# Kernel tuning notes

Hardware: AMD Instinct MI355X
Metric: run time of the kernel (lower is better)

Reference implementation:

```python
import jax, jax.numpy as jnp
import numpy as np

H = 1024
L = 2

def setup_inputs() -> dict:
    key = jax.random.key(0)
    k1, k2, k3, k4, k5 = jax.random.split(key, 5)
    B, S = 32, 2048
    scale = 1.0 / np.sqrt(H)
    return {
        "query": jax.random.normal(k1, (B, 1, H * L), dtype=jnp.float32),
        "keys": jax.random.normal(k2, (B, S, H), dtype=jnp.float32),
        "Wa_w": jax.random.normal(k3, (H * L, H), dtype=jnp.float32) * scale,
        "Wa_b": jnp.zeros((H,), dtype=jnp.float32),
        "Ua_w": jax.random.normal(k4, (H, H), dtype=jnp.float32) * scale,
        "Ua_b": jnp.zeros((H,), dtype=jnp.float32),
        "Va_w": jax.random.normal(k5, (H, 1), dtype=jnp.float32) * scale,
        "Va_b": jnp.zeros((1,), dtype=jnp.float32),
    }

def reference(query, keys, Wa_w, Wa_b, Ua_w, Ua_b, Va_w, Va_b):
    # query: [B,1,H*L], keys: [B,S,H]
    q = jnp.einsum('bqd,dh->bqh', query, Wa_w) + Wa_b   # [B,1,H]
    k = jnp.einsum('bsd,dh->bsh', keys, Ua_w) + Ua_b    # [B,S,H]
    e = jnp.tanh(q + k)                                  # [B,S,H]
    scores = jnp.einsum('bsh,ho->bso', e, Va_w) + Va_b   # [B,S,1]
    scores = scores[:, :, 0][:, None, :]                 # [B,1,S]
    weights = jax.nn.softmax(scores, axis=-1)            # [B,1,S]
    context = jnp.einsum('bqs,bsh->bqh', weights, keys)  # [B,1,H]
    return (context, weights)
```

## Files before the change

kernel.cpp:

```cpp
#include <hip/hip_runtime.h>
#include <hip/hip_bf16.h>


typedef __attribute__((ext_vector_type(8))) short short8;
typedef __attribute__((ext_vector_type(4))) float floatx4;

typedef const __attribute__((address_space(1))) unsigned int gu32;
typedef __attribute__((address_space(3))) unsigned int lu32;

__device__ __forceinline__ unsigned short f2bf(float f) {
    union { float f; unsigned int u; } c; c.f = f;
    unsigned int u = c.u + 0x7fffu + ((c.u >> 16) & 1u);
    return (unsigned short)(u >> 16);
}

__device__ __forceinline__ unsigned int f2bf2(float lo, float hi) {
#if __has_builtin(__builtin_amdgcn_cvt_pk_bf16_f32)
    auto r = __builtin_amdgcn_cvt_pk_bf16_f32(lo, hi);
    unsigned int u; __builtin_memcpy(&u, &r, 4);
    return u;
#else
    return (unsigned int)f2bf(lo) | ((unsigned int)f2bf(hi) << 16);
#endif
}

__device__ __forceinline__ void gld16(const void* g, const void* l) {
    __builtin_amdgcn_global_load_lds(
        (gu32*)(uintptr_t)g,
        (lu32*)(unsigned int)(uintptr_t)l,
        16, 0, 0);
}

__global__ __launch_bounds__(256) void prep_k(
    const float* __restrict__ query, const float* __restrict__ Wa,
    const float* __restrict__ Wab, const float* __restrict__ Uab,
    const float* __restrict__ Ua,
    float* __restrict__ qws, unsigned short* __restrict__ uat)
{
    const int tid = threadIdx.x;
    if (blockIdx.x < 512) {
        __shared__ float qs[2048];
        __shared__ float red[16*64];
        const int b = blockIdx.x >> 4, hc = blockIdx.x & 15;
        #pragma unroll
        for (int i = 0; i < 8; i++) qs[tid + 256*i] = query[b*2048 + tid + 256*i];
        __syncthreads();
        const int hq = tid & 15;
        const int dg = tid >> 4;
        const float4* wp = reinterpret_cast<const float4*>(Wa + (size_t)(dg*128)*1024 + hc*64 + hq*4);
        const float* qp = qs + dg*128;
        float4 a0; a0.x = a0.y = a0.z = a0.w = 0.f;
        float4 a1; a1.x = a1.y = a1.z = a1.w = 0.f;
        #pragma unroll 4
        for (int d = 0; d < 128; d += 2) {
            float q0 = qp[d], q1 = qp[d+1];
            float4 w0 = wp[(size_t)d*256];
            float4 w1 = wp[(size_t)(d+1)*256];
            a0.x += q0*w0.x; a0.y += q0*w0.y; a0.z += q0*w0.z; a0.w += q0*w0.w;
            a1.x += q1*w1.x; a1.y += q1*w1.y; a1.z += q1*w1.z; a1.w += q1*w1.w;
        }
        a0.x += a1.x; a0.y += a1.y; a0.z += a1.z; a0.w += a1.w;
        *reinterpret_cast<float4*>(red + dg*64 + hq*4) = a0;
        __syncthreads();
        if (tid < 64) {
            float v = 0.f;
            #pragma unroll
            for (int g = 0; g < 16; g++) v += red[g*64 + tid];
            int hh = hc*64 + tid;
            qws[b*1024 + hh] = v + Wab[hh] + Uab[hh];
        }
    } else {
        __shared__ unsigned short t[64][65];
        const int q = blockIdx.x - 512;
        const int x = tid & 63, yy = tid >> 6;
        const int d0 = (q >> 4)*64, h0 = (q & 15)*64;
        #pragma unroll
        for (int i = 0; i < 16; i++) {
            int y = yy*16 + i;
            t[y][x] = f2bf(Ua[(size_t)(d0+y)*1024 + h0 + x]);
        }
        __syncthreads();
        #pragma unroll
        for (int i = 0; i < 16; i++) {
            int y = yy*16 + i;
            uat[(size_t)(h0+y)*1024 + d0 + x] = t[x][y];
        }
    }
}

__global__ __launch_bounds__(256) void score_gemm_fast(
    const float* __restrict__ keys,
    const unsigned short* __restrict__ uat,
    const float* __restrict__ qws,
    const float* __restrict__ Va,
    float* __restrict__ score)
{
    __shared__ float          aSf[2][128*32];
    __shared__ unsigned short bS[2][256*32];
    const int tid = threadIdx.x;
    const int b  = blockIdx.z;
    const int s0 = blockIdx.x * 128;
    const int h0 = blockIdx.y * 256;
    const int lane = tid & 63, wave = tid >> 6;
    const int quad = lane >> 4, l15 = lane & 15;
    const int wm = (wave & 1) * 64, wn = (wave >> 1) * 128;

    const int srow = lane >> 2;
    const int schunk = (lane & 3) ^ ((srow >> 1) & 3);
    const unsigned short* ubase = uat + (size_t)h0*1024;
    size_t boff[4];
    #pragma unroll
    for (int u = 0; u < 4; u++) {
        int cg = wave*4 + u;
        boff[u] = (size_t)(cg*16 + srow)*1024 + schunk*8;
    }

    const float* kA = keys + (size_t)(b*2048 + s0)*1024;
    const int arow = tid >> 3;
    const int acx  = (tid & 7) ^ ((tid >> 3) & 7);
    size_t aoff[4];
    #pragma unroll
    for (int i = 0; i < 4; i++)
        aoff[i] = (size_t)(i*32 + arow)*1024 + acx*4;

    floatx4 acc[4][8];
    #pragma unroll
    for (int i = 0; i < 4; i++)
        #pragma unroll
        for (int j = 0; j < 8; j++) acc[i][j] = (floatx4)0.0f;

    #pragma unroll
    for (int i = 0; i < 4; i++)
        gld16(kA + aoff[i], (unsigned short*)aSf[0] + i*2048 + wave*512);
    #pragma unroll
    for (int u = 0; u < 4; u++)
        gld16(ubase + boff[u], bS[0] + (wave*4 + u)*512);
    __syncthreads();

    int cur = 0;
    for (int kt = 0; kt < 31; ++kt) {
        const int nxt = cur ^ 1;
        const int k1 = (kt + 1) << 5;

        #pragma unroll
        for (int i = 0; i < 4; i++)
            gld16(kA + aoff[i] + k1, (unsigned short*)aSf[nxt] + i*2048 + wave*512);
        #pragma unroll
        for (int u = 0; u < 4; u++)
            gld16(ubase + boff[u] + k1, bS[nxt] + (wave*4 + u)*512);

        short8 af[4], bf8[8];
        #pragma unroll
        for (int i = 0; i < 4; i++) {
            int row = wm + 16*i + l15;
            const float* rp = aSf[cur] + row*32;
            float4 v0 = *reinterpret_cast<const float4*>(rp + (((2*quad)   ^ (row&7)) * 4));
            float4 v1 = *reinterpret_cast<const float4*>(rp + (((2*quad+1) ^ (row&7)) * 4));
            union { uint4 u; short8 s; } cv;
            cv.u.x = f2bf2(v0.x, v0.y); cv.u.y = f2bf2(v0.z, v0.w);
            cv.u.z = f2bf2(v1.x, v1.y); cv.u.w = f2bf2(v1.z, v1.w);
            af[i] = cv.s;
        }
        #pragma unroll
        for (int j = 0; j < 8; j++) {
            int row = wn + 16*j + l15;
            bf8[j] = *reinterpret_cast<const short8*>(bS[cur] + row*32 + ((quad ^ ((row>>1)&3)) * 8));
        }
        #pragma unroll
        for (int i = 0; i < 4; i++)
            #pragma unroll
            for (int j = 0; j < 8; j++)
                acc[i][j] = __builtin_amdgcn_mfma_f32_16x16x32_bf16(af[i], bf8[j], acc[i][j], 0, 0, 0);

        __syncthreads();
        cur = nxt;
    }

    {
        short8 af[4], bf8[8];
        #pragma unroll
        for (int i = 0; i < 4; i++) {
            int row = wm + 16*i + l15;
            const float* rp = aSf[cur] + row*32;
            float4 v0 = *reinterpret_cast<const float4*>(rp + (((2*quad)   ^ (row&7)) * 4));
            float4 v1 = *reinterpret_cast<const float4*>(rp + (((2*quad+1) ^ (row&7)) * 4));
            union { uint4 u; short8 s; } cv;
            cv.u.x = f2bf2(v0.x, v0.y); cv.u.y = f2bf2(v0.z, v0.w);
            cv.u.z = f2bf2(v1.x, v1.y); cv.u.w = f2bf2(v1.z, v1.w);
            af[i] = cv.s;
        }
        #pragma unroll
        for (int j = 0; j < 8; j++) {
            int row = wn + 16*j + l15;
            bf8[j] = *reinterpret_cast<const short8*>(bS[cur] + row*32 + ((quad ^ ((row>>1)&3)) * 8));
        }
        #pragma unroll
        for (int i = 0; i < 4; i++)
            #pragma unroll
            for (int j = 0; j < 8; j++)
                acc[i][j] = __builtin_amdgcn_mfma_f32_16x16x32_bf16(af[i], bf8[j], acc[i][j], 0, 0, 0);
    }

    float qv[8], vav[8];
    #pragma unroll
    for (int j = 0; j < 8; j++) {
        int n = h0 + wn + 16*j + l15;
        qv[j]  = qws[b*1024 + n];
        vav[j] = Va[n];
    }
    #pragma unroll
    for (int i = 0; i < 4; i++) {
        #pragma unroll
        for (int r = 0; r < 4; r++) {
            float p = 0.f;
            #pragma unroll
            for (int j = 0; j < 8; j++) {
                float x = qv[j] + acc[i][j][r];
                float e = __expf(2.f * x);
                float t = 1.f - 2.f * __builtin_amdgcn_rcpf(e + 1.f);
                p += vav[j] * t;
            }
            #pragma unroll
            for (int off = 1; off < 16; off <<= 1) p += __shfl_xor(p, off, 64);
            if (l15 == 0) {
                int m = wm + 16*i + quad*4 + r;
                atomicAdd(score + (size_t)b*2048 + s0 + m, p);
            }
        }
    }
}

__global__ __launch_bounds__(256) void softmax_k(const float* __restrict__ score,
                                                 float* __restrict__ out_w)
{
    const int tid = threadIdx.x;
    const int b = blockIdx.x;
    __shared__ float wred[4], wred2[4];
    float sc[8];
    float mx = -3.0e38f;
    #pragma unroll
    for (int i = 0; i < 8; i++) {
        sc[i] = score[(size_t)b*2048 + tid + 256*i];
        mx = fmaxf(mx, sc[i]);
    }
    #pragma unroll
    for (int off = 32; off >= 1; off >>= 1) mx = fmaxf(mx, __shfl_xor(mx, off, 64));
    if ((tid & 63) == 0) wred[tid >> 6] = mx;
    __syncthreads();
    mx = fmaxf(fmaxf(wred[0], wred[1]), fmaxf(wred[2], wred[3]));
    float e[8]; float lsum = 0.f;
    #pragma unroll
    for (int i = 0; i < 8; i++) { e[i] = __expf(sc[i] - mx); lsum += e[i]; }
    #pragma unroll
    for (int off = 32; off >= 1; off >>= 1) lsum += __shfl_xor(lsum, off, 64);
    if ((tid & 63) == 0) wred2[tid >> 6] = lsum;
    __syncthreads();
    float inv = 1.0f / (wred2[0] + wred2[1] + wred2[2] + wred2[3]);
    #pragma unroll
    for (int i = 0; i < 8; i++) out_w[b*2048 + tid + 256*i] = e[i] * inv;
}

__global__ __launch_bounds__(256) void ctx_k(const float* __restrict__ keys,
                                             const float* __restrict__ w,
                                             float* __restrict__ out_ctx, int sper)
{
    const int tid = threadIdx.x;
    const int b = blockIdx.x, sc = blockIdx.y;
    const float4* k4 = reinterpret_cast<const float4*>(keys) + (size_t)(b*2048 + sc*sper)*256;
    const float* wp = w + b*2048 + sc*sper;
    float4 a; a.x = a.y = a.z = a.w = 0.f;
    #pragma unroll 4
    for (int s = 0; s < sper; s++) {
        float wv = wp[s];
        float4 kv = k4[(size_t)s*256 + tid];
        a.x += wv*kv.x; a.y += wv*kv.y; a.z += wv*kv.z; a.w += wv*kv.w;
    }
    float* o = out_ctx + (size_t)b*1024 + tid*4;
    atomicAdd(o + 0, a.x);
    atomicAdd(o + 1, a.y);
    atomicAdd(o + 2, a.z);
    atomicAdd(o + 3, a.w);
}

extern "C" void kernel_launch(void* const* d_in, const int* in_sizes, int n_in,
                              void* d_out, int out_size, void* d_ws, size_t ws_size,
                              hipStream_t stream)
{
    const float* query = (const float*)d_in[0];
    const float* keys  = (const float*)d_in[1];
    const float* Wa_w  = (const float*)d_in[2];
    const float* Wa_b  = (const float*)d_in[3];
    const float* Ua_w  = (const float*)d_in[4];
    const float* Ua_b  = (const float*)d_in[5];
    const float* Va_w  = (const float*)d_in[6];

    char* ws = (char*)d_ws;
    float*          qws   = (float*)(ws);
    unsigned short* uat   = (unsigned short*)(ws + 131072);
    float*          score = (float*)(ws + 131072 + 2097152);

    float* out_ctx = (float*)d_out;
    float* out_w   = out_ctx + 32*1024;

    hipMemsetAsync(score, 0, 32*2048*sizeof(float), stream);
    hipMemsetAsync(out_ctx, 0, 32*1024*sizeof(float), stream);
    prep_k<<<dim3(768), 256, 0, stream>>>(query, Wa_w, Wa_b, Ua_b, Ua_w, qws, uat);
    score_gemm_fast<<<dim3(16, 4, 32), 256, 0, stream>>>(keys, uat, qws, Va_w, score);
    softmax_k<<<dim3(32),     256, 0, stream>>>(score, out_w);
    ctx_k    <<<dim3(32, 16), 256, 0, stream>>>(keys, out_w, out_ctx, 128);
}
```

Measured before the change: 678.6 us.

## Shrink score GEMM N-tile to 128, relayout A smem, widen ctx grid

The score GEMM tile along H drops from 256 to 128 columns, so the grid doubles to 16x8x32 blocks and each wave keeps 4x4 instead of 4x8 accumulators. The fp32 keys tile in shared memory is split into two 16-column halves with a new XOR swizzle, which changes both the load mapping and the fragment reads. The context kernel now runs on a 32x64 grid with 32 rows per block, and the prep kernel's shared buffers are merged into one union. The aim is more occupancy and parallelism from fewer registers and smaller LDS per block, at the cost of reading the keys twice as often and doing twice as many score atomics.

```diff
diff --git a/kernel.cpp b/kernel.cpp
--- a/kernel.cpp
+++ b/kernel.cpp
@@ -31,16 +31,17 @@
         16, 0, 0);
 }
 
-__global__ __launch_bounds__(256) void prep_k(
+__global__ __launch_bounds__(256) void pre_k(
     const float* __restrict__ query, const float* __restrict__ Wa,
     const float* __restrict__ Wab, const float* __restrict__ Uab,
     const float* __restrict__ Ua,
     float* __restrict__ qws, unsigned short* __restrict__ uat)
 {
+    __shared__ char smem[12288];
     const int tid = threadIdx.x;
     if (blockIdx.x < 512) {
-        __shared__ float qs[2048];
-        __shared__ float red[16*64];
+        float* qs  = (float*)smem;
+        float* red = (float*)(smem + 8192);
         const int b = blockIdx.x >> 4, hc = blockIdx.x & 15;
         #pragma unroll
         for (int i = 0; i < 8; i++) qs[tid + 256*i] = query[b*2048 + tid + 256*i];
@@ -70,7 +71,8 @@
             qws[b*1024 + hh] = v + Wab[hh] + Uab[hh];
         }
     } else {
-        __shared__ unsigned short t[64][65];
+        typedef unsigned short row_t[65];
+        row_t* t = (row_t*)smem;
         const int q = blockIdx.x - 512;
         const int x = tid & 63, yy = tid >> 6;
         const int d0 = (q >> 4)*64, h0 = (q & 15)*64;
@@ -96,45 +98,44 @@
     float* __restrict__ score)
 {
     __shared__ float          aSf[2][128*32];
-    __shared__ unsigned short bS[2][256*32];
+    __shared__ unsigned short bS[2][128*32];
     const int tid = threadIdx.x;
     const int b  = blockIdx.z;
     const int s0 = blockIdx.x * 128;
-    const int h0 = blockIdx.y * 256;
+    const int h0 = blockIdx.y * 128;
     const int lane = tid & 63, wave = tid >> 6;
     const int quad = lane >> 4, l15 = lane & 15;
-    const int wm = (wave & 1) * 64, wn = (wave >> 1) * 128;
+    const int wm = (wave & 1) * 64, wn = (wave >> 1) * 64;
 
     const int srow = lane >> 2;
     const int schunk = (lane & 3) ^ ((srow >> 1) & 3);
+    const int c0 = wave*2, c1 = wave*2 + 1;
     const unsigned short* ubase = uat + (size_t)h0*1024;
-    size_t boff[4];
-    #pragma unroll
-    for (int u = 0; u < 4; u++) {
-        int cg = wave*4 + u;
-        boff[u] = (size_t)(cg*16 + srow)*1024 + schunk*8;
-    }
+    const size_t boff0 = (size_t)(c0*16 + srow)*1024 + schunk*8;
+    const size_t boff1 = (size_t)(c1*16 + srow)*1024 + schunk*8;
 
     const float* kA = keys + (size_t)(b*2048 + s0)*1024;
-    const int arow = tid >> 3;
-    const int acx  = (tid & 7) ^ ((tid >> 3) & 7);
+    const int arh = tid >> 2;
+    const int ac4 = (tid & 3) ^ ((tid >> 3) & 3);
     size_t aoff[4];
     #pragma unroll
+    for (int it = 0; it < 4; it++)
+        aoff[it] = (size_t)((it & 1)*64 + arh)*1024 + (size_t)(it >> 1)*16 + ac4*4;
+
+    floatx4 acc[4][4];
+    #pragma unroll
     for (int i = 0; i < 4; i++)
-        aoff[i] = (size_t)(i*32 + arow)*1024 + acx*4;
-
-    floatx4 acc[4][8];
-    #pragma unroll
-    for (int i = 0; i < 4; i++)
-        #pragma unroll
-        for (int j = 0; j < 8; j++) acc[i][j] = (floatx4)0.0f;
-
-    #pragma unroll
-    for (int i = 0; i < 4; i++)
-        gld16(kA + aoff[i], (unsigned short*)aSf[0] + i*2048 + wave*512);
-    #pragma unroll
-    for (int u = 0; u < 4; u++)
-        gld16(ubase + boff[u], bS[0] + (wave*4 + u)*512);
+        #pragma unroll
+        for (int j = 0; j < 4; j++) acc[i][j] = (floatx4)0.0f;
+
+    const int fst = (quad >> 1) * 2048;
+    const int cb  = (2*quad) & 3;
+
+    #pragma unroll
+    for (int it = 0; it < 4; it++)
+        gld16(kA + aoff[it], (unsigned short*)aSf[0] + it*2048 + wave*512);
+    gld16(ubase + boff0, bS[0] + c0*512);
+    gld16(ubase + boff1, bS[0] + c1*512);
     __syncthreads();
 
     int cur = 0;
@@ -143,33 +144,33 @@
         const int k1 = (kt + 1) << 5;
 
         #pragma unroll
-        for (int i = 0; i < 4; i++)
-            gld16(kA + aoff[i] + k1, (unsigned short*)aSf[nxt] + i*2048 + wave*512);
-        #pragma unroll
-        for (int u = 0; u < 4; u++)
-            gld16(ubase + boff[u] + k1, bS[nxt] + (wave*4 + u)*512);
-
-        short8 af[4], bf8[8];
+        for (int it = 0; it < 4; it++)
+            gld16(kA + aoff[it] + k1, (unsigned short*)aSf[nxt] + it*2048 + wave*512);
+        gld16(ubase + boff0 + k1, bS[nxt] + c0*512);
+        gld16(ubase + boff1 + k1, bS[nxt] + c1*512);
+
+        short8 af[4], bf8[4];
         #pragma unroll
         for (int i = 0; i < 4; i++) {
             int row = wm + 16*i + l15;
-            const float* rp = aSf[cur] + row*32;
-            float4 v0 = *reinterpret_cast<const float4*>(rp + (((2*quad)   ^ (row&7)) * 4));
-            float4 v1 = *reinterpret_cast<const float4*>(rp + (((2*quad+1) ^ (row&7)) * 4));
+            int rr  = (row >> 1) & 3;
+            const float* sub = aSf[cur] + fst + row*16;
+            float4 v0 = *reinterpret_cast<const float4*>(sub + ((cb ^ rr) << 2));
+            float4 v1 = *reinterpret_cast<const float4*>(sub + (((cb + 1) ^ rr) << 2));
             union { uint4 u; short8 s; } cv;
             cv.u.x = f2bf2(v0.x, v0.y); cv.u.y = f2bf2(v0.z, v0.w);
             cv.u.z = f2bf2(v1.x, v1.y); cv.u.w = f2bf2(v1.z, v1.w);
             af[i] = cv.s;
         }
         #pragma unroll
-        for (int j = 0; j < 8; j++) {
+        for (int j = 0; j < 4; j++) {
             int row = wn + 16*j + l15;
             bf8[j] = *reinterpret_cast<const short8*>(bS[cur] + row*32 + ((quad ^ ((row>>1)&3)) * 8));
         }
         #pragma unroll
         for (int i = 0; i < 4; i++)
             #pragma unroll
-            for (int j = 0; j < 8; j++)
+            for (int j = 0; j < 4; j++)
                 acc[i][j] = __builtin_amdgcn_mfma_f32_16x16x32_bf16(af[i], bf8[j], acc[i][j], 0, 0, 0);
 
         __syncthreads();
@@ -177,33 +178,34 @@
     }
 
     {
-        short8 af[4], bf8[8];
+        short8 af[4], bf8[4];
         #pragma unroll
         for (int i = 0; i < 4; i++) {
             int row = wm + 16*i + l15;
-            const float* rp = aSf[cur] + row*32;
-            float4 v0 = *reinterpret_cast<const float4*>(rp + (((2*quad)   ^ (row&7)) * 4));
-            float4 v1 = *reinterpret_cast<const float4*>(rp + (((2*quad+1) ^ (row&7)) * 4));
+            int rr  = (row >> 1) & 3;
+            const float* sub = aSf[cur] + fst + row*16;
+            float4 v0 = *reinterpret_cast<const float4*>(sub + ((cb ^ rr) << 2));
+            float4 v1 = *reinterpret_cast<const float4*>(sub + (((cb + 1) ^ rr) << 2));
             union { uint4 u; short8 s; } cv;
             cv.u.x = f2bf2(v0.x, v0.y); cv.u.y = f2bf2(v0.z, v0.w);
             cv.u.z = f2bf2(v1.x, v1.y); cv.u.w = f2bf2(v1.z, v1.w);
             af[i] = cv.s;
         }
         #pragma unroll
-        for (int j = 0; j < 8; j++) {
+        for (int j = 0; j < 4; j++) {
             int row = wn + 16*j + l15;
             bf8[j] = *reinterpret_cast<const short8*>(bS[cur] + row*32 + ((quad ^ ((row>>1)&3)) * 8));
         }
         #pragma unroll
         for (int i = 0; i < 4; i++)
             #pragma unroll
-            for (int j = 0; j < 8; j++)
+            for (int j = 0; j < 4; j++)
                 acc[i][j] = __builtin_amdgcn_mfma_f32_16x16x32_bf16(af[i], bf8[j], acc[i][j], 0, 0, 0);
     }
 
-    float qv[8], vav[8];
-    #pragma unroll
-    for (int j = 0; j < 8; j++) {
+    float qv[4], vav[4];
+    #pragma unroll
+    for (int j = 0; j < 4; j++) {
         int n = h0 + wn + 16*j + l15;
         qv[j]  = qws[b*1024 + n];
         vav[j] = Va[n];
@@ -214,7 +216,7 @@
         for (int r = 0; r < 4; r++) {
             float p = 0.f;
             #pragma unroll
-            for (int j = 0; j < 8; j++) {
+            for (int j = 0; j < 4; j++) {
                 float x = qv[j] + acc[i][j][r];
                 float e = __expf(2.f * x);
                 float t = 1.f - 2.f * __builtin_amdgcn_rcpf(e + 1.f);
@@ -304,8 +306,8 @@
 
     hipMemsetAsync(score, 0, 32*2048*sizeof(float), stream);
     hipMemsetAsync(out_ctx, 0, 32*1024*sizeof(float), stream);
-    prep_k<<<dim3(768), 256, 0, stream>>>(query, Wa_w, Wa_b, Ua_b, Ua_w, qws, uat);
-    score_gemm_fast<<<dim3(16, 4, 32), 256, 0, stream>>>(keys, uat, qws, Va_w, score);
+    pre_k<<<dim3(768), 256, 0, stream>>>(query, Wa_w, Wa_b, Ua_b, Ua_w, qws, uat);
+    score_gemm_fast<<<dim3(16, 8, 32), 256, 0, stream>>>(keys, uat, qws, Va_w, score);
     softmax_k<<<dim3(32),     256, 0, stream>>>(score, out_w);
-    ctx_k    <<<dim3(32, 16), 256, 0, stream>>>(keys, out_w, out_ctx, 128);
-}
+    ctx_k    <<<dim3(32, 64), 256, 0, stream>>>(keys, out_w, out_ctx, 32);
+}
```

Result: slower. 774.9 us (+14.2%).
